# Kernel tuning notes

Hardware: AMD Instinct MI355X
Metric: run time of the kernel (lower is better)

The kernel has to match this reference:

```python
import jax, jax.numpy as jnp
import numpy as np


def setup_inputs() -> dict:
    key = jax.random.key(0)
    k1, k2, k3, k4 = jax.random.split(key, 4)
    B, H, N, D = 4, 16, 2048, 128
    return {
        "q": jax.random.normal(k1, (B, H, N, D), dtype=jnp.float32),
        "k": jax.random.normal(k2, (B, H, N, D), dtype=jnp.float32),
        "v": jax.random.normal(k3, (B, H, N, D), dtype=jnp.float32),
        "g": jax.random.normal(k4, (B, H, N, 1), dtype=jnp.float32),
    }


def reference(q, k, v, g):
    """GLA recurrence: S_t = l_t * S_{t-1} + (1 - l_t) * k_t v_t^T; o_t = q_t S_t."""
    scale = 1.0
    B, H, N, D = q.shape
    lambd = jax.nn.sigmoid(g)                      # [B,H,N,1]
    qs = q * scale
    # time-major for scan: [N,B,H,...]
    qt = jnp.moveaxis(qs, 2, 0)
    kt = jnp.moveaxis(k, 2, 0)
    vt = jnp.moveaxis(v, 2, 0)
    lt = jnp.moveaxis(lambd, 2, 0)[..., None]      # [N,B,H,1,1]
    S0 = jnp.zeros((B, H, D, D), dtype=q.dtype)

    def step(S, inp):
        q_t, k_t, v_t, l_t = inp
        kv = jnp.einsum('bhd,bhe->bhde', k_t, v_t)  # rank-1 update per head
        S = l_t * S + (1.0 - l_t) * kv
        o = jnp.einsum('bhd,bhde->bhe', q_t, S)
        return S, o

    _, outs = jax.lax.scan(step, S0, (qt, kt, vt, lt))  # outs: [N,B,H,D]
    return jnp.moveaxis(outs, 0, 2)                     # [B,H,N,D]
```

## Files before the change

### kernel.cpp

```cpp
#include <hip/hip_runtime.h>

#define BH   64
#define NTOK 2048
#define DD   128
#define CHK  64
#define NCH  32

typedef __attribute__((ext_vector_type(8))) short bf16x8;
typedef __attribute__((ext_vector_type(4))) float f32x4;
typedef unsigned short u16;

__device__ __forceinline__ u16 f2bf(float f){
  union { float f; unsigned u; } x; x.f = f;
  unsigned r = (x.u + 0x7fffu + ((x.u >> 16) & 1u)) >> 16;
  return (u16)r;
}
__device__ __forceinline__ float bf2f(u16 h){
  union { unsigned u; float f; } x; x.u = ((unsigned)h) << 16;
  return x.f;
}
__device__ __forceinline__ int swz(int r, int c, int re){
  int b = (r*re + c)*2;
  return b ^ ((r & 7) << 4);
}
__device__ __forceinline__ void lds_w1(u16* a, int r, int c, int re, u16 v){
  *(u16*)((char*)a + swz(r,c,re)) = v;
}
__device__ __forceinline__ void lds_w4(u16* a, int r, int c, int re, ushort4 v){
  *(ushort4*)((char*)a + swz(r,c,re)) = v;
}
__device__ __forceinline__ bf16x8 lds_r8(const u16* a, int r, int c, int re){
  return *(const bf16x8*)((const char*)a + swz(r,c,re));
}

__global__ __launch_bounds__(256) void gla_k1(
    const float* __restrict__ Kg, const float* __restrict__ Vg,
    const float* __restrict__ Gg, u16* __restrict__ U, float* __restrict__ Ad)
{
  __shared__ float sb[CHK], sw[CHK];
  __shared__ u16 KbT[DD*CHK];
  __shared__ u16 VbT[DD*CHK];
  const int tid = threadIdx.x;
  const int bh = blockIdx.x >> 5, c = blockIdx.x & 31;
  const size_t tok0 = (size_t)bh*NTOK + (size_t)c*CHK;

  if (tid < 64){
    float gv = Gg[tok0 + tid];
    float l = 1.f/(1.f + expf(-gv));
    float x = log2f(l);
    #pragma unroll
    for (int off=1; off<64; off<<=1){
      float y = __shfl_up(x, off, 64);
      if (tid >= off) x += y;
    }
    sb[tid] = x;
    sw[tid] = 1.f - l;
  }
  __syncthreads();
  const float b63 = sb[CHK-1];

  {
    const int s = tid >> 2, d0 = (tid & 3) * 32;
    const float ck = exp2f(b63 - sb[s]) * sw[s];
    const float4* kp = (const float4*)(Kg + (tok0 + s)*DD + d0);
    const float4* vp = (const float4*)(Vg + (tok0 + s)*DD + d0);
    #pragma unroll
    for (int i=0;i<8;++i){
      float4 kf = kp[i], vf = vp[i];
      int d = d0 + i*4;
      lds_w1(KbT, d+0, s, CHK, f2bf(kf.x*ck));
      lds_w1(KbT, d+1, s, CHK, f2bf(kf.y*ck));
      lds_w1(KbT, d+2, s, CHK, f2bf(kf.z*ck));
      lds_w1(KbT, d+3, s, CHK, f2bf(kf.w*ck));
      lds_w1(VbT, d+0, s, CHK, f2bf(vf.x));
      lds_w1(VbT, d+1, s, CHK, f2bf(vf.y));
      lds_w1(VbT, d+2, s, CHK, f2bf(vf.z));
      lds_w1(VbT, d+3, s, CHK, f2bf(vf.w));
    }
  }
  __syncthreads();

  const int w = tid >> 6, l = tid & 63, lr = l & 15, lh = l >> 4;
  f32x4 acc[2][8] = {};
  #pragma unroll
  for (int ks=0; ks<2; ++ks){
    const int kk = ks*32 + lh*8;
    bf16x8 a0 = lds_r8(VbT, w*32 + lr,      kk, CHK);
    bf16x8 a1 = lds_r8(VbT, w*32 + 16 + lr, kk, CHK);
    #pragma unroll
    for (int n=0;n<8;++n){
      bf16x8 bb = lds_r8(KbT, n*16 + lr, kk, CHK);
      acc[0][n] = __builtin_amdgcn_mfma_f32_16x16x32_bf16(a0, bb, acc[0][n], 0,0,0);
      acc[1][n] = __builtin_amdgcn_mfma_f32_16x16x32_bf16(a1, bb, acc[1][n], 0,0,0);
    }
  }

  u16* Ug = U + ((size_t)blockIdx.x << 14);
  #pragma unroll
  for (int mi=0;mi<2;++mi)
    #pragma unroll
    for (int n=0;n<8;++n)
      #pragma unroll
      for (int r=0;r<4;++r){
        int e = w*32 + mi*16 + lh*4 + r;
        int d = n*16 + lr;
        Ug[e*DD + d] = f2bf(acc[mi][n][r]);
      }
  if (tid == 0) Ad[blockIdx.x] = exp2f(b63);
}

__global__ __launch_bounds__(256) void gla_k2(u16* __restrict__ U, const float* __restrict__ Ad)
{
  const int flat = blockIdx.x * 256 + threadIdx.x;
  const int bh  = flat >> 14;
  const int idx = flat & 16383;
  u16* p = U + ((size_t)bh << 19) + idx;
  const float* Ab = Ad + bh*NCH;
  float S = 0.f;
  #pragma unroll 4
  for (int c=0;c<NCH;++c){
    float u = bf2f(p[(size_t)c << 14]);
    p[(size_t)c << 14] = f2bf(S);
    S = fmaf(Ab[c], S, u);
  }
}

__global__ __launch_bounds__(256) void gla_k3(
    const float* __restrict__ Qg, const float* __restrict__ Kg,
    const float* __restrict__ Vg, const float* __restrict__ Gg,
    const u16* __restrict__ Sp, float* __restrict__ Og)
{
  __shared__ float sb[CHK], sw[CHK];
  __shared__ u16 Qb[CHK*DD];
  __shared__ u16 buf[DD*DD];
  __shared__ u16 Pb[CHK*CHK];
  const int tid = threadIdx.x;
  const int bh = blockIdx.x >> 5, c = blockIdx.x & 31;
  const size_t tok0 = (size_t)bh*NTOK + (size_t)c*CHK;

  if (tid < 64){
    float gv = Gg[tok0 + tid];
    float l = 1.f/(1.f + expf(-gv));
    float x = log2f(l);
    #pragma unroll
    for (int off=1; off<64; off<<=1){
      float y = __shfl_up(x, off, 64);
      if (tid >= off) x += y;
    }
    sb[tid] = x;
    sw[tid] = 1.f - l;
  }
  __syncthreads();

  const int rw = tid >> 2, d0 = (tid & 3)*32;
  {
    const float cq = exp2f(sb[rw]);
    const float4* qp = (const float4*)(Qg + (tok0 + rw)*DD + d0);
    #pragma unroll
    for (int i=0;i<8;++i){
      float4 f = qp[i];
      ushort4 u4 = make_ushort4(f2bf(f.x*cq), f2bf(f.y*cq), f2bf(f.z*cq), f2bf(f.w*cq));
      lds_w4(Qb, rw, d0 + i*4, DD, u4);
    }
  }
  {
    const int e = tid >> 1, dd = (tid & 1)*64;
    const ushort4* sp4 = (const ushort4*)(Sp + ((size_t)blockIdx.x << 14) + e*DD + dd);
    #pragma unroll
    for (int i=0;i<16;++i) lds_w4(buf, e, dd + i*4, DD, sp4[i]);
  }
  __syncthreads();

  const int w = tid >> 6, l = tid & 63, lr = l & 15, lh = l >> 4;
  f32x4 acc[8] = {};
  #pragma unroll
  for (int ks=0;ks<4;++ks){
    const int kk = ks*32 + lh*8;
    bf16x8 a = lds_r8(Qb, w*16 + lr, kk, DD);
    #pragma unroll
    for (int n=0;n<8;++n){
      bf16x8 bb = lds_r8(buf, n*16 + lr, kk, DD);
      acc[n] = __builtin_amdgcn_mfma_f32_16x16x32_bf16(a, bb, acc[n], 0,0,0);
    }
  }
  __syncthreads();

  u16* Kh = buf;
  u16* VT = buf + CHK*DD;
  {
    const float chk = exp2f(-sb[rw]) * sw[rw];
    const float4* kp = (const float4*)(Kg + (tok0 + rw)*DD + d0);
    const float4* vp = (const float4*)(Vg + (tok0 + rw)*DD + d0);
    #pragma unroll
    for (int i=0;i<8;++i){
      float4 kf = kp[i], vf = vp[i];
      int d = d0 + i*4;
      ushort4 u4 = make_ushort4(f2bf(kf.x*chk), f2bf(kf.y*chk), f2bf(kf.z*chk), f2bf(kf.w*chk));
      lds_w4(Kh, rw, d, DD, u4);
      lds_w1(VT, d+0, rw, CHK, f2bf(vf.x));
      lds_w1(VT, d+1, rw, CHK, f2bf(vf.y));
      lds_w1(VT, d+2, rw, CHK, f2bf(vf.z));
      lds_w1(VT, d+3, rw, CHK, f2bf(vf.w));
    }
  }
  __syncthreads();

  f32x4 pacc[4] = {};
  #pragma unroll
  for (int ks=0;ks<4;++ks){
    const int kk = ks*32 + lh*8;
    bf16x8 a = lds_r8(Qb, w*16 + lr, kk, DD);
    #pragma unroll
    for (int n=0;n<4;++n){
      bf16x8 bb = lds_r8(Kh, n*16 + lr, kk, DD);
      pacc[n] = __builtin_amdgcn_mfma_f32_16x16x32_bf16(a, bb, pacc[n], 0,0,0);
    }
  }
  #pragma unroll
  for (int n=0;n<4;++n)
    #pragma unroll
    for (int r=0;r<4;++r){
      int tt = w*16 + lh*4 + r;
      int ss = n*16 + lr;
      float pv = (ss <= tt) ? pacc[n][r] : 0.f;
      lds_w1(Pb, tt, ss, CHK, f2bf(pv));
    }
  __syncthreads();

  #pragma unroll
  for (int ks=0;ks<2;++ks){
    const int kk = ks*32 + lh*8;
    bf16x8 a = lds_r8(Pb, w*16 + lr, kk, CHK);
    #pragma unroll
    for (int n=0;n<8;++n){
      bf16x8 bb = lds_r8(VT, n*16 + lr, kk, CHK);
      acc[n] = __builtin_amdgcn_mfma_f32_16x16x32_bf16(a, bb, acc[n], 0,0,0);
    }
  }

  float* Op = Og + tok0*DD;
  #pragma unroll
  for (int n=0;n<8;++n)
    #pragma unroll
    for (int r=0;r<4;++r){
      int tt = w*16 + lh*4 + r;
      int e  = n*16 + lr;
      Op[tt*DD + e] = acc[n][r];
    }
}

extern "C" void kernel_launch(void* const* d_in, const int* in_sizes, int n_in,
                              void* d_out, int out_size, void* d_ws, size_t ws_size,
                              hipStream_t stream)
{
  const float* q = (const float*)d_in[0];
  const float* k = (const float*)d_in[1];
  const float* v = (const float*)d_in[2];
  const float* g = (const float*)d_in[3];
  float* out = (float*)d_out;
  u16*   U   = (u16*)d_ws;
  float* Ad  = (float*)((char*)d_ws + (size_t)BH*NCH*DD*DD*2);

  gla_k1<<<dim3(BH*NCH), dim3(256), 0, stream>>>(k, v, g, U, Ad);
  gla_k2<<<dim3(BH*DD*DD/256), dim3(256), 0, stream>>>(U, Ad);
  gla_k3<<<dim3(BH*NCH), dim3(256), 0, stream>>>(q, k, v, g, U, out);
}
```

Before: 132.3 us.

## Fuse chunked GLA into single persistent kernel with register-resident state

Replaces the three-kernel pipeline (per-chunk KV outer products, a separate inter-chunk scan, and an output kernel) with one kernel. Each block owns a head and a 32-column value slice and walks the chunks sequentially, keeping its running state in MFMA accumulators. K, V and gate data are prefetched into LDS asynchronously for the next chunk. This removes the large bf16 state workspace round trip and two launches. In exchange it launches only 256 blocks, serialises 32 chunk steps per block, and rereads Q and K once per value slice.

```diff
diff --git a/kernel.cpp b/kernel.cpp
--- a/kernel.cpp
+++ b/kernel.cpp
@@ -1,23 +1,21 @@
 #include <hip/hip_runtime.h>
 
-#define BH   64
 #define NTOK 2048
 #define DD   128
 #define CHK  64
 #define NCH  32
+#define EW   32
 
 typedef __attribute__((ext_vector_type(8))) short bf16x8;
 typedef __attribute__((ext_vector_type(4))) float f32x4;
 typedef unsigned short u16;
+typedef unsigned int u32;
+
+#define MFMA(a,b,c) __builtin_amdgcn_mfma_f32_16x16x32_bf16(a,b,c,0,0,0)
 
 __device__ __forceinline__ u16 f2bf(float f){
   union { float f; unsigned u; } x; x.f = f;
-  unsigned r = (x.u + 0x7fffu + ((x.u >> 16) & 1u)) >> 16;
-  return (u16)r;
-}
-__device__ __forceinline__ float bf2f(u16 h){
-  union { unsigned u; float f; } x; x.u = ((unsigned)h) << 16;
-  return x.f;
+  return (u16)((x.u + 0x7fffu + ((x.u >> 16) & 1u)) >> 16);
 }
 __device__ __forceinline__ int swz(int r, int c, int re){
   int b = (r*re + c)*2;
@@ -32,221 +30,183 @@
 __device__ __forceinline__ bf16x8 lds_r8(const u16* a, int r, int c, int re){
   return *(const bf16x8*)((const char*)a + swz(r,c,re));
 }
-
-__global__ __launch_bounds__(256) void gla_k1(
-    const float* __restrict__ Kg, const float* __restrict__ Vg,
-    const float* __restrict__ Gg, u16* __restrict__ U, float* __restrict__ Ad)
+__device__ __forceinline__ void gld16(const float* g, float* l){
+  __builtin_amdgcn_global_load_lds((const __attribute__((address_space(1))) u32*)g,
+                                   (__attribute__((address_space(3))) u32*)l, 16, 0, 0);
+}
+__device__ __forceinline__ void gld4(const float* g, float* l){
+  __builtin_amdgcn_global_load_lds((const __attribute__((address_space(1))) u32*)g,
+                                   (__attribute__((address_space(3))) u32*)l, 4, 0, 0);
+}
+
+__global__ __launch_bounds__(256) void gla_fused(
+    const float* __restrict__ Qg, const float* __restrict__ Kg,
+    const float* __restrict__ Vg, const float* __restrict__ Gg,
+    float* __restrict__ Og)
 {
-  __shared__ float sb[CHK], sw[CHK];
-  __shared__ u16 KbT[DD*CHK];
-  __shared__ u16 VbT[DD*CHK];
+  __shared__ float Kraw[CHK*DD];
+  __shared__ float Vraw[CHK*EW];
+  __shared__ float Graw[CHK];
+  __shared__ u16 Kh [CHK*DD];
+  __shared__ u16 KhT[DD*CHK];
+  __shared__ u16 VT [EW*CHK];
+  __shared__ u16 ST [EW*DD];
+  __shared__ u16 Pb [CHK*CHK];
+
   const int tid = threadIdx.x;
-  const int bh = blockIdx.x >> 5, c = blockIdx.x & 31;
-  const size_t tok0 = (size_t)bh*NTOK + (size_t)c*CHK;
-
-  if (tid < 64){
-    float gv = Gg[tok0 + tid];
-    float l = 1.f/(1.f + expf(-gv));
-    float x = log2f(l);
+  const int w = tid >> 6, l = tid & 63, lr = l & 15, lh = l >> 4;
+  const int slot = blockIdx.x >> 3;
+  const int bh = (blockIdx.x & 7) + 8*(slot >> 2);
+  const int e0 = (slot & 3) * EW;
+
+  const float* Qh  = Qg + (size_t)bh*NTOK*DD;
+  const float* Kgh = Kg + (size_t)bh*NTOK*DD;
+  const float* Vh  = Vg + (size_t)bh*NTOK*DD;
+  const float* Gh  = Gg + (size_t)bh*NTOK;
+  float* Oh = Og + (size_t)bh*NTOK*DD;
+
+  f32x4 S00 = {}, S01 = {}, S10 = {}, S11 = {};
+  float4 qpre[8];
+
+  auto prefetch = [&](int c){
+    const int t0 = c*CHK;
+    #pragma unroll
+    for (int i=0;i<8;++i){
+      int u = i*256 + tid;
+      int s = u >> 5, cu = u & 31;
+      int src = (cu & 24) | ((cu & 7) ^ (s & 7));
+      gld16(Kgh + (size_t)(t0+s)*DD + src*4, Kraw + u*4);
+    }
+    #pragma unroll
+    for (int i=0;i<2;++i){
+      int u = i*256 + tid;
+      int s = u >> 3, sub = u & 7;
+      gld16(Vh + (size_t)(t0+s)*DD + e0 + ((sub ^ (s&7))*4), Vraw + u*4);
+    }
+    if (w == 0) gld4(Gh + t0 + l, Graw + l);
+    const float* qp = Qh + (size_t)(t0 + w*16 + lr)*DD + lh*8;
+    #pragma unroll
+    for (int ks=0;ks<4;++ks){
+      qpre[ks*2]   = *(const float4*)(qp + ks*32);
+      qpre[ks*2+1] = *(const float4*)(qp + ks*32 + 4);
+    }
+  };
+
+  prefetch(0);
+
+  for (int c=0; c<NCH; ++c){
+    __syncthreads();
+
+    float gv = Graw[l];
+    float li = 1.f/(1.f + expf(-gv));
+    float x  = log2f(li);
     #pragma unroll
     for (int off=1; off<64; off<<=1){
       float y = __shfl_up(x, off, 64);
-      if (tid >= off) x += y;
-    }
-    sb[tid] = x;
-    sw[tid] = 1.f - l;
-  }
-  __syncthreads();
-  const float b63 = sb[CHK-1];
-
-  {
-    const int s = tid >> 2, d0 = (tid & 3) * 32;
-    const float ck = exp2f(b63 - sb[s]) * sw[s];
-    const float4* kp = (const float4*)(Kg + (tok0 + s)*DD + d0);
-    const float4* vp = (const float4*)(Vg + (tok0 + s)*DD + d0);
+      if (l >= off) x += y;
+    }
+    const float bl  = x;
+    const float ckl = exp2f(-bl) * (1.f - li);
+    const float cq  = exp2f(__shfl(bl, w*16 + lr, 64));
+    const float scc = exp2f(__shfl(bl, 63, 64));
+
     #pragma unroll
     for (int i=0;i<8;++i){
-      float4 kf = kp[i], vf = vp[i];
-      int d = d0 + i*4;
-      lds_w1(KbT, d+0, s, CHK, f2bf(kf.x*ck));
-      lds_w1(KbT, d+1, s, CHK, f2bf(kf.y*ck));
-      lds_w1(KbT, d+2, s, CHK, f2bf(kf.z*ck));
-      lds_w1(KbT, d+3, s, CHK, f2bf(kf.w*ck));
-      lds_w1(VbT, d+0, s, CHK, f2bf(vf.x));
-      lds_w1(VbT, d+1, s, CHK, f2bf(vf.y));
-      lds_w1(VbT, d+2, s, CHK, f2bf(vf.z));
-      lds_w1(VbT, d+3, s, CHK, f2bf(vf.w));
-    }
-  }
-  __syncthreads();
-
-  const int w = tid >> 6, l = tid & 63, lr = l & 15, lh = l >> 4;
-  f32x4 acc[2][8] = {};
-  #pragma unroll
-  for (int ks=0; ks<2; ++ks){
-    const int kk = ks*32 + lh*8;
-    bf16x8 a0 = lds_r8(VbT, w*32 + lr,      kk, CHK);
-    bf16x8 a1 = lds_r8(VbT, w*32 + 16 + lr, kk, CHK);
-    #pragma unroll
-    for (int n=0;n<8;++n){
-      bf16x8 bb = lds_r8(KbT, n*16 + lr, kk, CHK);
-      acc[0][n] = __builtin_amdgcn_mfma_f32_16x16x32_bf16(a0, bb, acc[0][n], 0,0,0);
-      acc[1][n] = __builtin_amdgcn_mfma_f32_16x16x32_bf16(a1, bb, acc[1][n], 0,0,0);
-    }
-  }
-
-  u16* Ug = U + ((size_t)blockIdx.x << 14);
-  #pragma unroll
-  for (int mi=0;mi<2;++mi)
-    #pragma unroll
-    for (int n=0;n<8;++n)
+      float4 kf = *(const float4*)(Kraw + l*DD + w*32 + ((i ^ (l&7)) * 4));
+      int d = w*32 + i*4;
+      u16 b0=f2bf(kf.x*ckl), b1=f2bf(kf.y*ckl), b2=f2bf(kf.z*ckl), b3=f2bf(kf.w*ckl);
+      lds_w4(Kh, l, d, DD, make_ushort4(b0,b1,b2,b3));
+      lds_w1(KhT, d+0, l, CHK, b0);
+      lds_w1(KhT, d+1, l, CHK, b1);
+      lds_w1(KhT, d+2, l, CHK, b2);
+      lds_w1(KhT, d+3, l, CHK, b3);
+    }
+    #pragma unroll
+    for (int j=0;j<2;++j){
+      float4 vf = *(const float4*)(Vraw + l*EW + (((w*2+j) ^ (l&7)) * 4));
+      int e = w*8 + j*4;
+      lds_w1(VT, e+0, l, CHK, f2bf(vf.x));
+      lds_w1(VT, e+1, l, CHK, f2bf(vf.y));
+      lds_w1(VT, e+2, l, CHK, f2bf(vf.z));
+      lds_w1(VT, e+3, l, CHK, f2bf(vf.w));
+    }
+    {
+      const int dbase = w*32 + lh*4;
       #pragma unroll
       for (int r=0;r<4;++r){
-        int e = w*32 + mi*16 + lh*4 + r;
-        int d = n*16 + lr;
-        Ug[e*DD + d] = f2bf(acc[mi][n][r]);
+        lds_w1(ST, lr,    dbase + r,      DD, f2bf(S00[r]));
+        lds_w1(ST, 16+lr, dbase + r,      DD, f2bf(S01[r]));
+        lds_w1(ST, lr,    dbase + 16 + r, DD, f2bf(S10[r]));
+        lds_w1(ST, 16+lr, dbase + 16 + r, DD, f2bf(S11[r]));
       }
-  if (tid == 0) Ad[blockIdx.x] = exp2f(b63);
-}
-
-__global__ __launch_bounds__(256) void gla_k2(u16* __restrict__ U, const float* __restrict__ Ad)
-{
-  const int flat = blockIdx.x * 256 + threadIdx.x;
-  const int bh  = flat >> 14;
-  const int idx = flat & 16383;
-  u16* p = U + ((size_t)bh << 19) + idx;
-  const float* Ab = Ad + bh*NCH;
-  float S = 0.f;
-  #pragma unroll 4
-  for (int c=0;c<NCH;++c){
-    float u = bf2f(p[(size_t)c << 14]);
-    p[(size_t)c << 14] = f2bf(S);
-    S = fmaf(Ab[c], S, u);
+    }
+    bf16x8 qA[4];
+    #pragma unroll
+    for (int ks=0;ks<4;++ks){
+      float4 a = qpre[ks*2], b = qpre[ks*2+1];
+      bf16x8 t;
+      t[0]=(short)f2bf(a.x*cq); t[1]=(short)f2bf(a.y*cq);
+      t[2]=(short)f2bf(a.z*cq); t[3]=(short)f2bf(a.w*cq);
+      t[4]=(short)f2bf(b.x*cq); t[5]=(short)f2bf(b.y*cq);
+      t[6]=(short)f2bf(b.z*cq); t[7]=(short)f2bf(b.w*cq);
+      qA[ks] = t;
+    }
+    __syncthreads();
+    if (c+1 < NCH) prefetch(c+1);
+
+    f32x4 oacc0 = {}, oacc1 = {};
+    f32x4 p0 = {}, p1 = {}, p2 = {}, p3 = {};
+    #pragma unroll
+    for (int ks=0;ks<4;++ks){
+      const int kk = ks*32 + lh*8;
+      bf16x8 a = qA[ks];
+      oacc0 = MFMA(a, lds_r8(ST, lr,    kk, DD), oacc0);
+      oacc1 = MFMA(a, lds_r8(ST, 16+lr, kk, DD), oacc1);
+      p0 = MFMA(a, lds_r8(Kh, lr,    kk, DD), p0);
+      p1 = MFMA(a, lds_r8(Kh, 16+lr, kk, DD), p1);
+      p2 = MFMA(a, lds_r8(Kh, 32+lr, kk, DD), p2);
+      p3 = MFMA(a, lds_r8(Kh, 48+lr, kk, DD), p3);
+    }
+    {
+      const int t = w*16 + lh*4;
+      #pragma unroll
+      for (int r=0;r<4;++r){
+        int tt = t + r;
+        lds_w1(Pb, tt, lr,    CHK, f2bf((lr    <= tt) ? p0[r] : 0.f));
+        lds_w1(Pb, tt, 16+lr, CHK, f2bf((16+lr <= tt) ? p1[r] : 0.f));
+        lds_w1(Pb, tt, 32+lr, CHK, f2bf((32+lr <= tt) ? p2[r] : 0.f));
+        lds_w1(Pb, tt, 48+lr, CHK, f2bf((48+lr <= tt) ? p3[r] : 0.f));
+      }
+    }
+    __syncthreads();
+
+    #pragma unroll
+    for (int k2=0;k2<2;++k2){
+      const int kk = k2*32 + lh*8;
+      bf16x8 vb0 = lds_r8(VT, lr,    kk, CHK);
+      bf16x8 vb1 = lds_r8(VT, 16+lr, kk, CHK);
+      bf16x8 pa  = lds_r8(Pb, w*16 + lr, kk, CHK);
+      oacc0 = MFMA(pa, vb0, oacc0);
+      oacc1 = MFMA(pa, vb1, oacc1);
+      bf16x8 ka0 = lds_r8(KhT, w*32 + lr,      kk, CHK);
+      bf16x8 ka1 = lds_r8(KhT, w*32 + 16 + lr, kk, CHK);
+      S00 = MFMA(ka0, vb0, S00);
+      S01 = MFMA(ka0, vb1, S01);
+      S10 = MFMA(ka1, vb0, S10);
+      S11 = MFMA(ka1, vb1, S11);
+    }
+    #pragma unroll
+    for (int r=0;r<4;++r){ S00[r]*=scc; S01[r]*=scc; S10[r]*=scc; S11[r]*=scc; }
+
+    {
+      float* op = Oh + (size_t)(c*CHK + w*16 + lh*4)*DD + e0;
+      #pragma unroll
+      for (int r=0;r<4;++r){
+        op[r*DD + lr]      = oacc0[r];
+        op[r*DD + 16 + lr] = oacc1[r];
+      }
+    }
   }
-}
-
-__global__ __launch_bounds__(256) void gla_k3(
-    const float* __restrict__ Qg, const float* __restrict__ Kg,
-    const float* __restrict__ Vg, const float* __restrict__ Gg,
-    const u16* __restrict__ Sp, float* __restrict__ Og)
-{
-  __shared__ float sb[CHK], sw[CHK];
-  __shared__ u16 Qb[CHK*DD];
-  __shared__ u16 buf[DD*DD];
-  __shared__ u16 Pb[CHK*CHK];
-  const int tid = threadIdx.x;
-  const int bh = blockIdx.x >> 5, c = blockIdx.x & 31;
-  const size_t tok0 = (size_t)bh*NTOK + (size_t)c*CHK;
-
-  if (tid < 64){
-    float gv = Gg[tok0 + tid];
-    float l = 1.f/(1.f + expf(-gv));
-    float x = log2f(l);
-    #pragma unroll
-    for (int off=1; off<64; off<<=1){
-      float y = __shfl_up(x, off, 64);
-      if (tid >= off) x += y;
-    }
-    sb[tid] = x;
-    sw[tid] = 1.f - l;
-  }
-  __syncthreads();
-
-  const int rw = tid >> 2, d0 = (tid & 3)*32;
-  {
-    const float cq = exp2f(sb[rw]);
-    const float4* qp = (const float4*)(Qg + (tok0 + rw)*DD + d0);
-    #pragma unroll
-    for (int i=0;i<8;++i){
-      float4 f = qp[i];
-      ushort4 u4 = make_ushort4(f2bf(f.x*cq), f2bf(f.y*cq), f2bf(f.z*cq), f2bf(f.w*cq));
-      lds_w4(Qb, rw, d0 + i*4, DD, u4);
-    }
-  }
-  {
-    const int e = tid >> 1, dd = (tid & 1)*64;
-    const ushort4* sp4 = (const ushort4*)(Sp + ((size_t)blockIdx.x << 14) + e*DD + dd);
-    #pragma unroll
-    for (int i=0;i<16;++i) lds_w4(buf, e, dd + i*4, DD, sp4[i]);
-  }
-  __syncthreads();
-
-  const int w = tid >> 6, l = tid & 63, lr = l & 15, lh = l >> 4;
-  f32x4 acc[8] = {};
-  #pragma unroll
-  for (int ks=0;ks<4;++ks){
-    const int kk = ks*32 + lh*8;
-    bf16x8 a = lds_r8(Qb, w*16 + lr, kk, DD);
-    #pragma unroll
-    for (int n=0;n<8;++n){
-      bf16x8 bb = lds_r8(buf, n*16 + lr, kk, DD);
-      acc[n] = __builtin_amdgcn_mfma_f32_16x16x32_bf16(a, bb, acc[n], 0,0,0);
-    }
-  }
-  __syncthreads();
-
-  u16* Kh = buf;
-  u16* VT = buf + CHK*DD;
-  {
-    const float chk = exp2f(-sb[rw]) * sw[rw];
-    const float4* kp = (const float4*)(Kg + (tok0 + rw)*DD + d0);
-    const float4* vp = (const float4*)(Vg + (tok0 + rw)*DD + d0);
-    #pragma unroll
-    for (int i=0;i<8;++i){
-      float4 kf = kp[i], vf = vp[i];
-      int d = d0 + i*4;
-      ushort4 u4 = make_ushort4(f2bf(kf.x*chk), f2bf(kf.y*chk), f2bf(kf.z*chk), f2bf(kf.w*chk));
-      lds_w4(Kh, rw, d, DD, u4);
-      lds_w1(VT, d+0, rw, CHK, f2bf(vf.x));
-      lds_w1(VT, d+1, rw, CHK, f2bf(vf.y));
-      lds_w1(VT, d+2, rw, CHK, f2bf(vf.z));
-      lds_w1(VT, d+3, rw, CHK, f2bf(vf.w));
-    }
-  }
-  __syncthreads();
-
-  f32x4 pacc[4] = {};
-  #pragma unroll
-  for (int ks=0;ks<4;++ks){
-    const int kk = ks*32 + lh*8;
-    bf16x8 a = lds_r8(Qb, w*16 + lr, kk, DD);
-    #pragma unroll
-    for (int n=0;n<4;++n){
-      bf16x8 bb = lds_r8(Kh, n*16 + lr, kk, DD);
-      pacc[n] = __builtin_amdgcn_mfma_f32_16x16x32_bf16(a, bb, pacc[n], 0,0,0);
-    }
-  }
-  #pragma unroll
-  for (int n=0;n<4;++n)
-    #pragma unroll
-    for (int r=0;r<4;++r){
-      int tt = w*16 + lh*4 + r;
-      int ss = n*16 + lr;
-      float pv = (ss <= tt) ? pacc[n][r] : 0.f;
-      lds_w1(Pb, tt, ss, CHK, f2bf(pv));
-    }
-  __syncthreads();
-
-  #pragma unroll
-  for (int ks=0;ks<2;++ks){
-    const int kk = ks*32 + lh*8;
-    bf16x8 a = lds_r8(Pb, w*16 + lr, kk, CHK);
-    #pragma unroll
-    for (int n=0;n<8;++n){
-      bf16x8 bb = lds_r8(VT, n*16 + lr, kk, CHK);
-      acc[n] = __builtin_amdgcn_mfma_f32_16x16x32_bf16(a, bb, acc[n], 0,0,0);
-    }
-  }
-
-  float* Op = Og + tok0*DD;
-  #pragma unroll
-  for (int n=0;n<8;++n)
-    #pragma unroll
-    for (int r=0;r<4;++r){
-      int tt = w*16 + lh*4 + r;
-      int e  = n*16 + lr;
-      Op[tt*DD + e] = acc[n][r];
-    }
 }
 
 extern "C" void kernel_launch(void* const* d_in, const int* in_sizes, int n_in,
@@ -258,10 +218,6 @@
   const float* v = (const float*)d_in[2];
   const float* g = (const float*)d_in[3];
   float* out = (float*)d_out;
-  u16*   U   = (u16*)d_ws;
-  float* Ad  = (float*)((char*)d_ws + (size_t)BH*NCH*DD*DD*2);
-
-  gla_k1<<<dim3(BH*NCH), dim3(256), 0, stream>>>(k, v, g, U, Ad);
-  gla_k2<<<dim3(BH*DD*DD/256), dim3(256), 0, stream>>>(U, Ad);
-  gla_k3<<<dim3(BH*NCH), dim3(256), 0, stream>>>(q, k, v, g, U, out);
-}
+
+  gla_fused<<<dim3(256), dim3(256), 0, stream>>>(q, k, v, g, out);
+}
```

After: 122.0 us. -7.8%, faster.
